# Kernel optimization log

Hardware: AMD Instinct MI355X
Metric: run time of the kernel (lower is better)

## Reference

```python
import jax, jax.numpy as jnp
import numpy as np

B, L, H, V = 256, 4096, 64, 64
LN_EPS = 1e-5


def setup_inputs() -> dict:
    key = jax.random.key(0)
    ks = jax.random.split(key, 12)
    s = 1.0 / np.sqrt(H)
    return {
        "seq": jax.random.randint(ks[0], (B, L), 0, V),
        "embed_W": jax.random.normal(ks[1], (V, H), jnp.float32),
        "ff_w1": jax.random.normal(ks[2], (H, 2 * H), jnp.float32) * s,
        "ff_b1": jnp.zeros((2 * H,), jnp.float32),
        "ff_w2": jax.random.normal(ks[3], (2 * H, H), jnp.float32) * s,
        "ff_b2": jnp.zeros((H,), jnp.float32),
        "ln_w": jnp.ones((H,), jnp.float32),
        "ln_b": jnp.zeros((H,), jnp.float32),
        "read_w": jax.random.normal(ks[4], (H, H), jnp.float32) * s,
        "read_b": jnp.zeros((H,), jnp.float32),
        "out_w": jax.random.normal(ks[5], (H, V), jnp.float32) * s,
        "out_b": jnp.zeros((V,), jnp.float32),
    }


def _layer_norm(x, w, b):
    mu = jnp.mean(x, axis=-1, keepdims=True)
    var = jnp.mean(jnp.square(x - mu), axis=-1, keepdims=True)
    return (x - mu) * jax.lax.rsqrt(var + LN_EPS) * w + b


def reference(seq, embed_W, ff_w1, ff_b1, ff_w2, ff_b2, ln_w, ln_b,
              read_w, read_b, out_w, out_b):
    h = embed_W[seq]  # (B, L, H)
    ff = jax.nn.relu(h @ ff_w1 + ff_b1) @ ff_w2 + ff_b2
    h = _layer_norm(h + ff, ln_w, ln_b)

    def step(M, k):  # M: (B,H,H), k: (B,H)
        v_pred = jnp.einsum('bij,bj->bi', M, k)
        denom = jnp.sum(k * k, axis=-1, keepdims=True) + 1e-6
        dv = k - v_pred / denom
        M = M + dv[:, :, None] * k[:, None, :]  # rank-1 delta write
        return M, None

    ks = jnp.swapaxes(h[:, :-1, :], 0, 1)  # (L-1, B, H)
    M0 = jnp.zeros((h.shape[0], h.shape[-1], h.shape[-1]), h.dtype)
    M, _ = jax.lax.scan(step, M0, ks)

    q = h[:, -1, :]
    ctx = jnp.einsum('bij,bj->bi', M, q)
    return (ctx @ read_w + read_b) @ out_w + out_b  # (B, V)
```

## Files before the change

### kernel.cpp

```cpp
#include <hip/hip_runtime.h>
#include <hip/hip_bf16.h>

#define LN_EPS 1e-5f

static __device__ __forceinline__ float readlane_f(float v, int lane) {
    return __int_as_float(__builtin_amdgcn_readlane(__float_as_int(v), lane));
}

__global__ __launch_bounds__(64) void build_keys(
    const float* __restrict__ embed,
    const float* __restrict__ w1,
    const float* __restrict__ b1,
    const float* __restrict__ w2,
    const float* __restrict__ b2,
    const float* __restrict__ lnw,
    const float* __restrict__ lnb,
    float* __restrict__ keytab)
{
    const int v = blockIdx.x, lane = threadIdx.x;
    __shared__ float se[64];
    __shared__ float sh[128];
    se[lane] = embed[v * 64 + lane];
    __syncthreads();
    float h0 = b1[lane];
    float h1 = b1[lane + 64];
    #pragma unroll 8
    for (int i = 0; i < 64; ++i) {
        float e = se[i];
        h0 = fmaf(e, w1[i * 128 + lane], h0);
        h1 = fmaf(e, w1[i * 128 + lane + 64], h1);
    }
    sh[lane]      = fmaxf(h0, 0.f);
    sh[lane + 64] = fmaxf(h1, 0.f);
    __syncthreads();
    float acc = b2[lane];
    #pragma unroll 8
    for (int j = 0; j < 128; ++j)
        acc = fmaf(sh[j], w2[j * 64 + lane], acc);
    float pre = se[lane] + acc;
    float sum = pre;
    #pragma unroll
    for (int off = 32; off >= 1; off >>= 1) sum += __shfl_xor(sum, off, 64);
    float mu  = sum * (1.f / 64.f);
    float dev = pre - mu;
    float sq  = dev * dev;
    #pragma unroll
    for (int off = 32; off >= 1; off >>= 1) sq += __shfl_xor(sq, off, 64);
    float var = sq * (1.f / 64.f);
    float key = dev * (1.f / sqrtf(var + LN_EPS)) * lnw[lane] + lnb[lane];
    keytab[v * 64 + lane] = key;
}

__global__ __launch_bounds__(64) void build_tables(
    const float* __restrict__ keytab,
    const float* __restrict__ read_w,
    const float* __restrict__ read_b,
    const float* __restrict__ out_w,
    const float* __restrict__ out_b,
    float* __restrict__ Gg,
    float* __restrict__ GhatN,
    float* __restrict__ Wc,
    float* __restrict__ biasv)
{
    const int w = blockIdx.x, lane = threadIdx.x;
    __shared__ float sk[64 * 65];
    __shared__ float srw[64];
    #pragma unroll 8
    for (int r = 0; r < 64; ++r) sk[r * 65 + lane] = keytab[r * 64 + lane];
    srw[lane] = read_w[w * 64 + lane];
    __syncthreads();
    float g = 0.f;
    #pragma unroll 8
    for (int i = 0; i < 64; ++i)
        g = fmaf(sk[w * 65 + i], sk[lane * 65 + i], g);
    float gww  = readlane_f(g, w);
    float beta = 1.f / (gww + 1e-6f);
    Gg[w * 64 + lane]    = g;
    GhatN[w * 64 + lane] = -(beta * g);
    float acc = 0.f;
    #pragma unroll 8
    for (int j = 0; j < 64; ++j)
        acc = fmaf(srw[j], out_w[j * 64 + lane], acc);
    Wc[w * 64 + lane] = acc;
    if (w == 0) {
        float bacc = out_b[lane];
        #pragma unroll 8
        for (int j = 0; j < 64; ++j)
            bacc = fmaf(read_b[j], out_w[j * 64 + lane], bacc);
        biasv[lane] = bacc;
    }
}

__global__ __launch_bounds__(64) void delta_scan(
    const int*   __restrict__ seq,
    const float* __restrict__ Gg,
    const float* __restrict__ GhatN,
    const float* __restrict__ keytab,
    const float* __restrict__ Wc,
    const float* __restrict__ biasv,
    float* __restrict__ out)
{
    const int lane = threadIdx.x;
    const int b    = blockIdx.x;
    __shared__ float sG[64 * 64];
    __shared__ float sC[64];
    __shared__ float sCtx[64];
    #pragma unroll 8
    for (int r = 0; r < 64; ++r) sG[r * 64 + lane] = GhatN[r * 64 + lane];
    const int* seqb = seq + (size_t)b * 4096;
    const int wq = seqb[4095];
    float d = Gg[wq * 64 + lane];
    __syncthreads();

    float c = 0.f, s1 = 0.f, gh1 = 0.f;
    int vcur = seqb[64 * 63 + lane];
    float q_[9];
    #pragma unroll
    for (int k = 0; k < 9; ++k) {
        int w = __builtin_amdgcn_readlane(vcur, 62 - k);
        q_[k] = sG[w * 64 + lane];
    }

    #pragma unroll 1
    for (int blk = 64; blk >= 0; --blk) {
        int vnext = (blk > 0) ? seqb[(blk - 1) * 63 + lane] : vcur;

        #pragma unroll
        for (int jb = 62; jb >= 17; jb -= 9) {
            int wg[9], wp[9];
            #pragma unroll
            for (int k = 0; k < 9; ++k) wg[k] = __builtin_amdgcn_readlane(vcur, jb - k);
            #pragma unroll
            for (int k = 0; k < 9; ++k) wp[k] = __builtin_amdgcn_readlane(vcur, jb - 9 - k);
            #pragma unroll
            for (int k = 0; k < 9; ++k) {
                float p  = readlane_f(d,   wg[k]);
                float g  = readlane_f(gh1, wg[k]);
                float s0 = fmaf(s1, g, p);
                d = fmaf(s1, gh1, d);
                c += (lane == wg[k]) ? s0 : 0.f;
                float rn = q_[k];
                q_[k] = sG[wp[k] * 64 + lane];
                s1 = s0; gh1 = rn;
            }
        }
        {
            int wg[9], wp[9];
            #pragma unroll
            for (int k = 0; k < 9; ++k) wg[k] = __builtin_amdgcn_readlane(vcur, 8 - k);
            #pragma unroll
            for (int k = 0; k < 9; ++k) wp[k] = __builtin_amdgcn_readlane(vnext, 62 - k);
            #pragma unroll
            for (int k = 0; k < 9; ++k) {
                float p  = readlane_f(d,   wg[k]);
                float g  = readlane_f(gh1, wg[k]);
                float s0 = fmaf(s1, g, p);
                d = fmaf(s1, gh1, d);
                c += (lane == wg[k]) ? s0 : 0.f;
                float rn = q_[k];
                q_[k] = sG[wp[k] * 64 + lane];
                s1 = s0; gh1 = rn;
            }
        }
        vcur = vnext;
    }

    sC[lane] = c;
    __syncthreads();
    float ctx = 0.f;
    #pragma unroll 8
    for (int v = 0; v < 64; ++v)
        ctx = fmaf(sC[v], keytab[v * 64 + lane], ctx);
    sCtx[lane] = ctx;
    __syncthreads();
    float o = biasv[lane];
    #pragma unroll 8
    for (int i = 0; i < 64; ++i)
        o = fmaf(sCtx[i], Wc[i * 64 + lane], o);
    out[(size_t)b * 64 + lane] = o;
}

extern "C" void kernel_launch(void* const* d_in, const int* in_sizes, int n_in,
                              void* d_out, int out_size, void* d_ws, size_t ws_size,
                              hipStream_t stream) {
    const int*   seq    = (const int*)d_in[0];
    const float* embed  = (const float*)d_in[1];
    const float* ff_w1  = (const float*)d_in[2];
    const float* ff_b1  = (const float*)d_in[3];
    const float* ff_w2  = (const float*)d_in[4];
    const float* ff_b2  = (const float*)d_in[5];
    const float* ln_w   = (const float*)d_in[6];
    const float* ln_b   = (const float*)d_in[7];
    const float* read_w = (const float*)d_in[8];
    const float* read_b = (const float*)d_in[9];
    const float* out_w  = (const float*)d_in[10];
    const float* out_b  = (const float*)d_in[11];
    float* out = (float*)d_out;

    float* wsf    = (float*)d_ws;
    float* keytab = wsf;
    float* Gg     = wsf + 4096;
    float* GhatN  = wsf + 8192;
    float* Wc     = wsf + 12288;
    float* biasv  = wsf + 16384;

    build_keys<<<64, 64, 0, stream>>>(embed, ff_w1, ff_b1, ff_w2, ff_b2, ln_w, ln_b, keytab);
    build_tables<<<64, 64, 0, stream>>>(keytab, read_w, read_b, out_w, out_b,
                                        Gg, GhatN, Wc, biasv);
    delta_scan<<<256, 64, 0, stream>>>(seq, Gg, GhatN, keytab, Wc, biasv, out);
}
```

Baseline: 199.3 us.

## Interleave two batch sequences per wavefront in delta scan for ILP

Each workgroup now runs the recurrent delta scan for two batch rows, interleaving their independent dependency chains step by step so the latency of readlane and LDS gathers in one chain can overlap with the other. The grid shrinks to half as many blocks, and the epilogue projections share loads of keytab and Wc across both rows. The trade-off is fewer workgroups than CUs and higher register pressure, in exchange for more instruction-level parallelism per wave.

Result: slower. 291.5 us (+46.3%).

```diff
diff --git a/kernel.cpp b/kernel.cpp
--- a/kernel.cpp
+++ b/kernel.cpp
@@ -101,83 +101,92 @@
     float* __restrict__ out)
 {
     const int lane = threadIdx.x;
-    const int b    = blockIdx.x;
+    const int bA   = 2 * blockIdx.x;
+    const int bB   = bA + 1;
     __shared__ float sG[64 * 64];
-    __shared__ float sC[64];
-    __shared__ float sCtx[64];
+    __shared__ float sC[2][64];
+    __shared__ float sCtx[2][64];
     #pragma unroll 8
     for (int r = 0; r < 64; ++r) sG[r * 64 + lane] = GhatN[r * 64 + lane];
-    const int* seqb = seq + (size_t)b * 4096;
-    const int wq = seqb[4095];
-    float d = Gg[wq * 64 + lane];
-    __syncthreads();
-
-    float c = 0.f, s1 = 0.f, gh1 = 0.f;
-    int vcur = seqb[64 * 63 + lane];
-    float q_[9];
+    const int* seqA = seq + (size_t)bA * 4096;
+    const int* seqB = seq + (size_t)bB * 4096;
+    float dA = Gg[seqA[4095] * 64 + lane];
+    float dB = Gg[seqB[4095] * 64 + lane];
+    __syncthreads();
+
+    float cA = 0.f, sA = 0.f, ghA = 0.f;
+    float cB = 0.f, sB = 0.f, ghB = 0.f;
+    int vcA = seqA[64 * 63 + lane];
+    int vcB = seqB[64 * 63 + lane];
+    float qA[9], qB[9];
     #pragma unroll
     for (int k = 0; k < 9; ++k) {
-        int w = __builtin_amdgcn_readlane(vcur, 62 - k);
-        q_[k] = sG[w * 64 + lane];
+        int wa = __builtin_amdgcn_readlane(vcA, 62 - k);
+        int wb = __builtin_amdgcn_readlane(vcB, 62 - k);
+        qA[k] = sG[wa * 64 + lane];
+        qB[k] = sG[wb * 64 + lane];
     }
 
     #pragma unroll 1
     for (int blk = 64; blk >= 0; --blk) {
-        int vnext = (blk > 0) ? seqb[(blk - 1) * 63 + lane] : vcur;
-
+        int vnA = (blk > 0) ? seqA[(blk - 1) * 63 + lane] : vcA;
+        int vnB = (blk > 0) ? seqB[(blk - 1) * 63 + lane] : vcB;
         #pragma unroll
-        for (int jb = 62; jb >= 17; jb -= 9) {
-            int wg[9], wp[9];
-            #pragma unroll
-            for (int k = 0; k < 9; ++k) wg[k] = __builtin_amdgcn_readlane(vcur, jb - k);
-            #pragma unroll
-            for (int k = 0; k < 9; ++k) wp[k] = __builtin_amdgcn_readlane(vcur, jb - 9 - k);
-            #pragma unroll
-            for (int k = 0; k < 9; ++k) {
-                float p  = readlane_f(d,   wg[k]);
-                float g  = readlane_f(gh1, wg[k]);
-                float s0 = fmaf(s1, g, p);
-                d = fmaf(s1, gh1, d);
-                c += (lane == wg[k]) ? s0 : 0.f;
-                float rn = q_[k];
-                q_[k] = sG[wp[k] * 64 + lane];
-                s1 = s0; gh1 = rn;
+        for (int j = 62; j >= 0; --j) {
+            const int slot = (62 - j) % 9;
+            const int jl   = j - 9;
+            {
+                int   w0 = __builtin_amdgcn_readlane(vcA, j);
+                float p  = readlane_f(dA,  w0);
+                float g  = readlane_f(ghA, w0);
+                float s0 = fmaf(sA, g, p);
+                dA = fmaf(sA, ghA, dA);
+                cA += (lane == w0) ? s0 : 0.f;
+                float rn = qA[slot];
+                int wpre = (jl >= 0) ? __builtin_amdgcn_readlane(vcA, jl)
+                                     : __builtin_amdgcn_readlane(vnA, jl + 63);
+                qA[slot] = sG[wpre * 64 + lane];
+                sA = s0; ghA = rn;
+            }
+            {
+                int   w0 = __builtin_amdgcn_readlane(vcB, j);
+                float p  = readlane_f(dB,  w0);
+                float g  = readlane_f(ghB, w0);
+                float s0 = fmaf(sB, g, p);
+                dB = fmaf(sB, ghB, dB);
+                cB += (lane == w0) ? s0 : 0.f;
+                float rn = qB[slot];
+                int wpre = (jl >= 0) ? __builtin_amdgcn_readlane(vcB, jl)
+                                     : __builtin_amdgcn_readlane(vnB, jl + 63);
+                qB[slot] = sG[wpre * 64 + lane];
+                sB = s0; ghB = rn;
             }
         }
-        {
-            int wg[9], wp[9];
-            #pragma unroll
-            for (int k = 0; k < 9; ++k) wg[k] = __builtin_amdgcn_readlane(vcur, 8 - k);
-            #pragma unroll
-            for (int k = 0; k < 9; ++k) wp[k] = __builtin_amdgcn_readlane(vnext, 62 - k);
-            #pragma unroll
-            for (int k = 0; k < 9; ++k) {
-                float p  = readlane_f(d,   wg[k]);
-                float g  = readlane_f(gh1, wg[k]);
-                float s0 = fmaf(s1, g, p);
-                d = fmaf(s1, gh1, d);
-                c += (lane == wg[k]) ? s0 : 0.f;
-                float rn = q_[k];
-                q_[k] = sG[wp[k] * 64 + lane];
-                s1 = s0; gh1 = rn;
-            }
-        }
-        vcur = vnext;
-    }
-
-    sC[lane] = c;
-    __syncthreads();
-    float ctx = 0.f;
-    #pragma unroll 8
-    for (int v = 0; v < 64; ++v)
-        ctx = fmaf(sC[v], keytab[v * 64 + lane], ctx);
-    sCtx[lane] = ctx;
-    __syncthreads();
-    float o = biasv[lane];
-    #pragma unroll 8
-    for (int i = 0; i < 64; ++i)
-        o = fmaf(sCtx[i], Wc[i * 64 + lane], o);
-    out[(size_t)b * 64 + lane] = o;
+        vcA = vnA; vcB = vnB;
+    }
+
+    sC[0][lane] = cA;
+    sC[1][lane] = cB;
+    __syncthreads();
+    float ctxA = 0.f, ctxB = 0.f;
+    #pragma unroll 8
+    for (int v = 0; v < 64; ++v) {
+        float kv = keytab[v * 64 + lane];
+        ctxA = fmaf(sC[0][v], kv, ctxA);
+        ctxB = fmaf(sC[1][v], kv, ctxB);
+    }
+    sCtx[0][lane] = ctxA;
+    sCtx[1][lane] = ctxB;
+    __syncthreads();
+    float oA = biasv[lane], oB = oA;
+    #pragma unroll 8
+    for (int i = 0; i < 64; ++i) {
+        float wv = Wc[i * 64 + lane];
+        oA = fmaf(sCtx[0][i], wv, oA);
+        oB = fmaf(sCtx[1][i], wv, oB);
+    }
+    out[(size_t)bA * 64 + lane] = oA;
+    out[(size_t)bB * 64 + lane] = oB;
 }
 
 extern "C" void kernel_launch(void* const* d_in, const int* in_sizes, int n_in,
@@ -207,5 +216,5 @@
     build_keys<<<64, 64, 0, stream>>>(embed, ff_w1, ff_b1, ff_w2, ff_b2, ln_w, ln_b, keytab);
     build_tables<<<64, 64, 0, stream>>>(keytab, read_w, read_b, out_w, out_b,
                                         Gg, GhatN, Wc, biasv);
-    delta_scan<<<256, 64, 0, stream>>>(seq, Gg, GhatN, keytab, Wc, biasv, out);
-}
+    delta_scan<<<128, 64, 0, stream>>>(seq, Gg, GhatN, keytab, Wc, biasv, out);
+}
```
